# Kernel optimization log

Hardware: AMD Instinct MI355X
Metric: run time of the kernel (lower is better)

## Reference

```python
import jax, jax.numpy as jnp
import numpy as np

B, HIMG, WIMG = 8, 24, 24
WIDTH, NCH, CW = 1024, 8, 128
NHEADS, HD = 8, 16
HALF = HD // 2
NFREQ, VOCAB, NCLS = 32, 256, 10
HIDDEN = 4096
EPS = 1e-6
LAMBDA_INIT = 0.8 - 0.6 * float(np.exp(-0.3 * 0.0))  # layer_idx = 0


def rmsnorm(x, w, eps=EPS):
    return x * jax.lax.rsqrt(jnp.mean(x * x, axis=-1, keepdims=True) + eps) * w


def causal_attn(q, k, v, scale):
    # q,k: [B,H,L,d2], v: [B,H,L,D]
    L = q.shape[2]
    scores = jnp.einsum('bhqd,bhkd->bhqk', q, k) * scale
    mask = jnp.tril(jnp.ones((L, L), dtype=bool))
    scores = jnp.where(mask, scores, -jnp.inf)
    return jnp.einsum('bhqk,bhkd->bhqd', jax.nn.softmax(scores, axis=-1), v)


def diff_attn(h, qkv_w, qkv_b, qn_w, kn_w, hn_w, lq1, lk1, lq2, lk2, ow, ob):
    Bb, L, C = h.shape
    qkv = jax.nn.silu(h @ qkv_w + qkv_b).reshape(Bb, L, 3, NHEADS, HD)
    q, k, v = qkv[:, :, 0], qkv[:, :, 1], qkv[:, :, 2]
    t = lambda a: a.transpose(0, 2, 1, 3)  # [B,L,H,d] -> [B,H,L,d]
    q1 = t(rmsnorm(q[..., :HALF], qn_w)); q2 = t(rmsnorm(q[..., HALF:], qn_w))
    k1 = t(rmsnorm(k[..., :HALF], kn_w)); k2 = t(rmsnorm(k[..., HALF:], kn_w))
    v = t(v)
    lam = jnp.exp(jnp.dot(lq1, lk1)) - jnp.exp(jnp.dot(lq2, lk2)) + LAMBDA_INIT
    scale = 1.0 / np.sqrt(HALF)
    out1 = causal_attn(q1, k1, v, scale)
    out2 = causal_attn(q2, k2, v, scale)
    diff = rmsnorm(out1 - lam * out2, hn_w) * (1.0 - LAMBDA_INIT)
    out = diff.transpose(0, 2, 1, 3).reshape(Bb, L, C)
    return jax.nn.silu(out @ ow + ob)


def setup_inputs() -> dict:
    key = jax.random.key(0)
    ks = iter(jax.random.split(key, 64))
    n = lambda shape, s=0.02: jax.random.normal(next(ks), shape, jnp.float32) * s
    return dict(
        x=jax.random.uniform(next(ks), (B, HIMG, WIMG), jnp.float32),
        top_k=4,
        pixel_embed=n((VOCAB, WIDTH)),
        freq_h=n((NFREQ,), 0.1), freq_w=n((NFREQ,), 0.1),
        phase_h=jnp.zeros((NFREQ,), jnp.float32), phase_w=jnp.zeros((NFREQ,), jnp.float32),
        pos_proj_w=n((4 * NFREQ, WIDTH)), pos_proj_b=jnp.zeros((WIDTH,), jnp.float32),
        embed_norm_w=jnp.ones((WIDTH,), jnp.float32),
        se_w1=n((WIDTH, WIDTH // 4)), se_b1=jnp.zeros((WIDTH // 4,), jnp.float32),
        se_w2=n((WIDTH // 4, WIDTH)), se_b2=jnp.zeros((WIDTH,), jnp.float32),
        mix_norm_w=jnp.ones((WIDTH,), jnp.float32),
        mlp_w1=n((WIDTH, HIDDEN)), mlp_b1=jnp.zeros((HIDDEN,), jnp.float32),
        mlp_w2=n((HIDDEN, WIDTH)), mlp_b2=jnp.zeros((WIDTH,), jnp.float32),
        mlp_norm_w=jnp.ones((WIDTH,), jnp.float32),
        router_w=n((WIDTH, NCH)), router_b=jnp.zeros((NCH,), jnp.float32),
        qkv_w=n((NCH, CW, 3 * CW)), qkv_b=jnp.zeros((NCH, 3 * CW), jnp.float32),
        q_norm_w=jnp.ones((NCH, HALF), jnp.float32), k_norm_w=jnp.ones((NCH, HALF), jnp.float32),
        head_norm_w=jnp.ones((NCH, HD), jnp.float32),
        lam_q1=n((NCH, HALF), 0.1), lam_k1=n((NCH, HALF), 0.1),
        lam_q2=n((NCH, HALF), 0.1), lam_k2=n((NCH, HALF), 0.1),
        out_w=n((NCH, CW, CW)), out_b=jnp.zeros((NCH, CW), jnp.float32),
        seg_norm_w=jnp.ones((NCH, CW), jnp.float32),
        head_w=n((WIDTH, NCLS)), head_b=jnp.zeros((NCLS,), jnp.float32),
    )


def reference(x, top_k, pixel_embed, freq_h, freq_w, phase_h, phase_w, pos_proj_w,
              pos_proj_b, embed_norm_w, se_w1, se_b1, se_w2, se_b2, mix_norm_w,
              mlp_w1, mlp_b1, mlp_w2, mlp_b2, mlp_norm_w, router_w, router_b,
              qkv_w, qkv_b, q_norm_w, k_norm_w, head_norm_w, lam_q1, lam_k1,
              lam_q2, lam_k2, out_w, out_b, seg_norm_w, head_w, head_b):
    Bb, H, W = x.shape
    L = H * W
    # LearnedSinusoidal2DEmbed
    hp = jnp.arange(H, dtype=jnp.float32) / H
    wp = jnp.arange(W, dtype=jnp.float32) / W
    fh = jax.nn.softplus(freq_h) * 10.0
    fw = jax.nn.softplus(freq_w) * 10.0
    ha = hp[:, None] * fh + phase_h          # [H, NFREQ]
    wa = wp[:, None] * fw + phase_w
    h_enc = jnp.concatenate([jnp.sin(ha), jnp.cos(ha)], -1)
    w_enc = jnp.concatenate([jnp.sin(wa), jnp.cos(wa)], -1)
    pos = jnp.concatenate([jnp.broadcast_to(h_enc[:, None], (H, W, 2 * NFREQ)),
                           jnp.broadcast_to(w_enc[None, :], (H, W, 2 * NFREQ))], -1)
    pos = pos @ pos_proj_w + pos_proj_b      # [H, W, WIDTH]
    xi = jnp.clip((x * 255.0).astype(jnp.int32), 0, 255).reshape(Bb, L)
    h = pixel_embed[xi] + pos.reshape(1, L, WIDTH)
    h = rmsnorm(h, embed_norm_w)
    # ChannelMixer: SE + RMSNorm residual, MLP residual, top-k router
    s = jnp.mean(h, axis=1)
    s = jax.nn.sigmoid(jax.nn.silu(s @ se_w1 + se_b1) @ se_w2 + se_b2)
    h = h + rmsnorm(h * s[:, None, :] - h, mix_norm_w)
    h = h + rmsnorm(jax.nn.silu(h @ mlp_w1 + mlp_b1) @ mlp_w2 + mlp_b2, mlp_norm_w)
    logits_r = jnp.mean(h, axis=1) @ router_w + router_b   # [B, NCH]
    tv, ti = jax.lax.top_k(logits_r, top_k)
    rw = jnp.zeros_like(logits_r).at[jnp.arange(Bb)[:, None], ti].set(jax.nn.softmax(tv, axis=-1))
    # ChannelSegment: per-channel differential attention expert, routed
    outs = []
    for i in range(NCH):
        hi = h[..., i * CW:(i + 1) * CW]
        o = diff_attn(hi, qkv_w[i], qkv_b[i], q_norm_w[i], k_norm_w[i], head_norm_w[i],
                      lam_q1[i], lam_k1[i], lam_q2[i], lam_k2[i], out_w[i], out_b[i])
        hi = hi + rmsnorm(o, seg_norm_w[i])
        outs.append(hi * rw[:, i][:, None, None])
    h = jnp.concatenate(outs, axis=-1)
    # classifier head
    return jnp.mean(h, axis=1) @ head_w + head_b
```

## Files before the change

### kernel.cpp

```cpp
#include <hip/hip_runtime.h>
#include <math.h>

typedef __bf16 bf16;
typedef __bf16 bf16x8 __attribute__((ext_vector_type(8)));
typedef __bf16 bf16x4 __attribute__((ext_vector_type(4)));
typedef __bf16 bf16x2 __attribute__((ext_vector_type(2)));
typedef float f32x4 __attribute__((ext_vector_type(4)));
typedef short s16x4 __attribute__((ext_vector_type(4)));

constexpr int Bsz = 8, HIMG = 24, WIMG = 24;
constexpr int Lq = 576;
constexpr int WIDTH = 1024, NCH = 8, CW = 128;
constexpr int NHEADS = 8, HD = 16, HALF = 8;
constexpr float EPS = 1e-6f;
constexpr float LAMINIT = 0.2f;
constexpr float QSCALE_E = 0.35355339059327373f * 1.4426950408889634f;
constexpr int ROWS = Bsz * Lq;

__device__ __forceinline__ float fexp2(float x) {
#if __has_builtin(__builtin_amdgcn_exp2f)
  return __builtin_amdgcn_exp2f(x);
#else
  return exp2f(x);
#endif
}

constexpr size_t B_HB    = 0;
constexpr size_t B_G2B   = B_HB    + 9437184;
constexpr size_t B_ENCB  = B_G2B   + 9437184;
constexpr size_t B_POSWT = B_ENCB  + 163840;
constexpr size_t B_QKVWT = B_POSWT + 262144;
constexpr size_t B_OWT   = B_QKVWT + 786432;
constexpr size_t B_SE    = B_OWT   + 262144;
constexpr size_t B_T1    = B_SE    + 32768;
constexpr size_t B_MP    = B_T1    + 8192;
constexpr size_t B_RW    = B_MP    + 524288;
constexpr size_t B_LAM   = B_RW    + 256;
constexpr size_t B_POOL  = B_LAM   + 256;

__device__ __forceinline__ float blockReduceSum256(float v, float* red) {
  #pragma unroll
  for (int off = 32; off; off >>= 1) v += __shfl_down(v, off, 64);
  int lane = threadIdx.x & 63, wid = threadIdx.x >> 6;
  if (lane == 0) red[wid] = v;
  __syncthreads();
  float total = 0.f;
  #pragma unroll
  for (int i = 0; i < 4; i++) total += red[i];
  return total;
}
__device__ __forceinline__ float silu(float x) { return x / (1.f + __expf(-x)); }

__device__ __forceinline__ void gl16(const bf16* g, bf16* l) {
  __builtin_amdgcn_global_load_lds(
      (const __attribute__((address_space(1))) void*)g,
      (__attribute__((address_space(3))) void*)l, 16, 0, 0);
}

__device__ __forceinline__ f32x4 mfma16(bf16x4 a, bf16x4 b, f32x4 c) {
#if __has_builtin(__builtin_amdgcn_mfma_f32_16x16x16bf16_1k)
  union { bf16x4 h; s16x4 s; } ua, ub;
  ua.h = a; ub.h = b;
  return __builtin_amdgcn_mfma_f32_16x16x16bf16_1k(ua.s, ub.s, c, 0, 0, 0);
#else
  f32x4 d = c;
  asm volatile("v_mfma_f32_16x16x16_bf16 %0, %1, %2, %0"
               : "+v"(d) : "v"(a), "v"(b));
  return d;
#endif
}

__global__ __launch_bounds__(256) void k_tcast(const float* __restrict__ W,
    bf16* __restrict__ Wt, int K, int N) {
  __shared__ float t[32][33];
  int n0 = blockIdx.x * 32, k0 = blockIdx.y * 32;
  long zo = (long)blockIdx.z * K * N;
  int tid = threadIdx.x;
  int r = tid >> 3, c4 = (tid & 7) * 4;
  const float4 v = *(const float4*)(W + zo + (long)(k0 + r) * N + n0 + c4);
  t[c4 + 0][r] = v.x; t[c4 + 1][r] = v.y; t[c4 + 2][r] = v.z; t[c4 + 3][r] = v.w;
  __syncthreads();
  bf16* dst = Wt + zo + (long)(n0 + r) * K + k0 + c4;
  dst[0] = (bf16)t[r][c4 + 0]; dst[1] = (bf16)t[r][c4 + 1];
  dst[2] = (bf16)t[r][c4 + 2]; dst[3] = (bf16)t[r][c4 + 3];
}

__global__ void k_enc_b(const float* __restrict__ fh, const float* __restrict__ fw,
                        const float* __restrict__ ph, const float* __restrict__ pw,
                        bf16* __restrict__ enc) {
  int idx = blockIdx.x * blockDim.x + threadIdx.x;
  if (idx >= Lq * 128) return;
  int l = idx >> 7, c = idx & 127;
  int hh = l / WIMG, ww = l % WIMG;
  float v;
  if (c < 64) {
    int f = c & 31;
    float fr = log1pf(__expf(fh[f])) * 10.f;
    float a = (hh / (float)HIMG) * fr + ph[f];
    v = (c < 32) ? sinf(a) : cosf(a);
  } else {
    int f = c & 31;
    float fr = log1pf(__expf(fw[f])) * 10.f;
    float a = (ww / (float)WIMG) * fr + pw[f];
    v = (c < 96) ? sinf(a) : cosf(a);
  }
  enc[idx] = (bf16)v;
}

template <int ACT, int OUTBF>
__global__ __launch_bounds__(256) void gemm_bt(
    const bf16* __restrict__ A, int lda, long aZs,
    const bf16* __restrict__ Bt, long bZs,
    const float* __restrict__ bias, int biasZs,
    void* __restrict__ Cv, int ldc, long cZs,
    int M, int N, int K) {
  __shared__ bf16 As[128 * 32];
  __shared__ bf16 Bs[128 * 32];
  int tid = threadIdx.x;
  int m0 = blockIdx.y * 128, n0 = blockIdx.x * 128;
  int z = blockIdx.z;
  const bf16* Ab = A + (long)z * aZs;
  const bf16* Bb = Bt + (long)z * bZs;
  f32x4 acc[4][4] = {};
  int wv = tid >> 6, lane = tid & 63;
  int wrow = (wv >> 1) * 64, wcol = (wv & 1) * 64;
  int lm = lane & 15, lq = lane >> 4;
  const bf16* ag = Ab + (long)(m0 + (tid >> 2)) * lda + (tid & 3) * 8;
  const bf16* bg = Bb + (long)(n0 + (tid >> 2)) * K + (tid & 3) * 8;
  bf16* asd = As + tid * 8;
  bf16* bsd = Bs + tid * 8;
  for (int k0 = 0; k0 < K; k0 += 32) {
    gl16(ag + k0, asd);
    gl16(ag + k0 + 64L * lda, asd + 2048);
    gl16(bg + k0, bsd);
    gl16(bg + k0 + 64L * K, bsd + 2048);
    __syncthreads();
    bf16x8 af[4], bfr[4];
    #pragma unroll
    for (int i = 0; i < 4; i++) {
      af[i]  = *(const bf16x8*)(As + (wrow + i * 16 + lm) * 32 + lq * 8);
      bfr[i] = *(const bf16x8*)(Bs + (wcol + i * 16 + lm) * 32 + lq * 8);
    }
    #pragma unroll
    for (int i = 0; i < 4; i++)
      #pragma unroll
      for (int j = 0; j < 4; j++)
        acc[i][j] = __builtin_amdgcn_mfma_f32_16x16x32_bf16(af[i], bfr[j], acc[i][j], 0, 0, 0);
    __syncthreads();
  }
  long cz = (long)z * cZs;
  const float* bz = bias ? bias + (long)z * biasZs : nullptr;
  #pragma unroll
  for (int i = 0; i < 4; i++) {
    int row = m0 + wrow + i * 16 + lq * 4;
    #pragma unroll
    for (int j = 0; j < 4; j++) {
      int col = n0 + wcol + j * 16 + lm;
      float bv = bz ? bz[col] : 0.f;
      #pragma unroll
      for (int r = 0; r < 4; r++) {
        float v = acc[i][j][r] + bv;
        if (ACT == 1) v = silu(v);
        long off = cz + (long)(row + r) * ldc + col;
        if (OUTBF) ((bf16*)Cv)[off] = (bf16)v;
        else       ((float*)Cv)[off] = v;
      }
    }
  }
}

template <int ACT, int OUTBF, int ACC>
__global__ __launch_bounds__(256) void gemm64(
    const bf16* __restrict__ A, int lda, long aZs,
    const bf16* __restrict__ Bt, int ldb, long bZs,
    const float* __restrict__ bias, int biasZs,
    void* __restrict__ Cv, int ldc, long cZs,
    int M, int N, int K) {
  __shared__ bf16 As[64 * 32];
  __shared__ bf16 Bs[128 * 32];
  int tid = threadIdx.x;
  int m0 = blockIdx.y * 64, n0 = blockIdx.x * 128;
  int z = blockIdx.z;
  const bf16* Ab = A + (long)z * aZs;
  const bf16* Bb = Bt + (long)z * bZs;
  f32x4 acc[4][2] = {};
  int wv = tid >> 6, lane = tid & 63;
  int lm = lane & 15, lq = lane >> 4;
  int wcol = wv * 32;
  const bf16* ag = Ab + (long)(m0 + (tid >> 2)) * lda + (tid & 3) * 8;
  const bf16* bg = Bb + (long)(n0 + (tid >> 2)) * ldb + (tid & 3) * 8;
  bf16* asd = As + tid * 8;
  bf16* bsd = Bs + tid * 8;
  for (int k0 = 0; k0 < K; k0 += 32) {
    if (tid < 256) gl16(ag + k0, asd);
    gl16(bg + k0, bsd);
    gl16(bg + k0 + 64L * ldb, bsd + 2048);
    __syncthreads();
    bf16x8 af[4], bfr[2];
    #pragma unroll
    for (int i = 0; i < 4; i++)
      af[i] = *(const bf16x8*)(As + (i * 16 + lm) * 32 + lq * 8);
    #pragma unroll
    for (int j = 0; j < 2; j++)
      bfr[j] = *(const bf16x8*)(Bs + (wcol + j * 16 + lm) * 32 + lq * 8);
    #pragma unroll
    for (int i = 0; i < 4; i++)
      #pragma unroll
      for (int j = 0; j < 2; j++)
        acc[i][j] = __builtin_amdgcn_mfma_f32_16x16x32_bf16(af[i], bfr[j], acc[i][j], 0, 0, 0);
    __syncthreads();
  }
  long cz = (long)z * cZs;
  const float* bz = bias ? bias + (long)z * biasZs : nullptr;
  #pragma unroll
  for (int i = 0; i < 4; i++) {
    int row = m0 + i * 16 + lq * 4;
    #pragma unroll
    for (int j = 0; j < 2; j++) {
      int col = n0 + wcol + j * 16 + lm;
      float bv = bz ? bz[col] : 0.f;
      #pragma unroll
      for (int r = 0; r < 4; r++) {
        float v = acc[i][j][r] + bv;
        long off = cz + (long)(row + r) * ldc + col;
        if (ACC) v += (float)((bf16*)Cv)[off];
        if (ACT == 1) v = silu(v);
        if (OUTBF) ((bf16*)Cv)[off] = (bf16)v;
        else       ((float*)Cv)[off] = v;
      }
    }
  }
}

__global__ __launch_bounds__(256) void k_embed(const float* __restrict__ x,
    const float* __restrict__ emb, const float* __restrict__ pos,
    const float* __restrict__ nw, bf16* __restrict__ h) {
  __shared__ float red[4];
  int row = blockIdx.x;
  int l = row % Lq;
  int xi = (int)(x[row] * 255.f);
  xi = min(max(xi, 0), 255);
  const float* er = emb + (long)xi * WIDTH;
  const float* pr = pos + (long)l * WIDTH;
  int c0 = threadIdx.x * 4;
  float v[4]; float ss = 0.f;
  #pragma unroll
  for (int i = 0; i < 4; i++) { v[i] = er[c0 + i] + pr[c0 + i]; ss += v[i] * v[i]; }
  ss = blockReduceSum256(ss, red);
  float r = rsqrtf(ss / WIDTH + EPS);
  bf16* hr = h + (long)row * WIDTH;
  #pragma unroll
  for (int i = 0; i < 4; i++) hr[c0 + i] = (bf16)(v[i] * r * nw[c0 + i]);
}

__global__ void k_meanl_p(const bf16* __restrict__ h, float* __restrict__ part) {
  int lp = blockIdx.x, b = blockIdx.y, t = threadIdx.x;
  const bf16* p = h + ((long)b * Lq + (long)lp * 36) * WIDTH + t * 4;
  float a0 = 0, a1 = 0, a2 = 0, a3 = 0;
  for (int l = 0; l < 36; l++) {
    bf16x4 v = *(const bf16x4*)(p + (long)l * WIDTH);
    a0 += (float)v[0]; a1 += (float)v[1]; a2 += (float)v[2]; a3 += (float)v[3];
  }
  float* dst = part + ((long)b * 16 + lp) * WIDTH + t * 4;
  dst[0] = a0; dst[1] = a1; dst[2] = a2; dst[3] = a3;
}

__global__ __launch_bounds__(256) void k_se1(const float* __restrict__ part,
    const float* __restrict__ w1, const float* __restrict__ b1,
    float* __restrict__ t1) {
  __shared__ float sv[1024];
  __shared__ float red[256];
  int jb = blockIdx.x, b = blockIdx.y, t = threadIdx.x;
  for (int c = t; c < 1024; c += 256) {
    float a = 0.f;
    #pragma unroll
    for (int lp = 0; lp < 16; lp++) a += part[((long)b * 16 + lp) * 1024 + c];
    sv[c] = a * (1.f / 576.f);
  }
  __syncthreads();
  int j = t & 7, pt = t >> 3;
  int j0 = jb * 8;
  float acc = 0.f;
  int c0 = pt * 32;
  #pragma unroll 8
  for (int c = c0; c < c0 + 32; c++) acc += sv[c] * w1[c * 256 + j0 + j];
  red[t] = acc;
  __syncthreads();
  if (t < 8) {
    float a = b1[j0 + t];
    #pragma unroll
    for (int p = 0; p < 32; p++) a += red[p * 8 + t];
    t1[b * 256 + j0 + t] = silu(a);
  }
}

__global__ __launch_bounds__(256) void k_se2(const float* __restrict__ t1,
    const float* __restrict__ w2, const float* __restrict__ b2,
    float* __restrict__ s) {
  __shared__ float red[256];
  int jb = blockIdx.x, b = blockIdx.y, t = threadIdx.x;
  int j = t & 31, pt = t >> 5;
  int j0 = jb * 32;
  const float* tb = t1 + b * 256;
  float acc = 0.f;
  int c0 = pt * 32;
  #pragma unroll 8
  for (int c = c0; c < c0 + 32; c++) acc += tb[c] * w2[c * 1024 + j0 + j];
  red[t] = acc;
  __syncthreads();
  if (t < 32) {
    float a = b2[j0 + t];
    #pragma unroll
    for (int p = 0; p < 8; p++) a += red[p * 32 + t];
    s[b * 1024 + j0 + t] = 1.f / (1.f + __expf(-a));
  }
}

__global__ __launch_bounds__(256) void k_mix_b(bf16* __restrict__ h,
    const float* __restrict__ s, const float* __restrict__ mw) {
  __shared__ float red[4];
  int row = blockIdx.x;
  int b = row / Lq;
  bf16* hr = h + (long)row * WIDTH;
  const float* sb = s + b * WIDTH;
  int c0 = threadIdx.x * 4;
  float hv[4], y[4]; float ss = 0.f;
  #pragma unroll
  for (int i = 0; i < 4; i++) {
    hv[i] = (float)hr[c0 + i];
    y[i] = hv[i] * (sb[c0 + i] - 1.f); ss += y[i] * y[i];
  }
  ss = blockReduceSum256(ss, red);
  float r = rsqrtf(ss / WIDTH + EPS);
  #pragma unroll
  for (int i = 0; i < 4; i++) hr[c0 + i] = (bf16)(hv[i] + y[i] * r * mw[c0 + i]);
}

__global__ __launch_bounds__(256) void k_addnorm_b(bf16* __restrict__ h,
    const bf16* __restrict__ g, const float* __restrict__ mw) {
  __shared__ float red[4];
  int row = blockIdx.x;
  bf16* hr = h + (long)row * WIDTH;
  const bf16* gr = g + (long)row * WIDTH;
  int c0 = threadIdx.x * 4;
  float y[4]; float ss = 0.f;
  #pragma unroll
  for (int i = 0; i < 4; i++) { y[i] = (float)gr[c0 + i]; ss += y[i] * y[i]; }
  ss = blockReduceSum256(ss, red);
  float r = rsqrtf(ss / WIDTH + EPS);
  #pragma unroll
  for (int i = 0; i < 4; i++)
    hr[c0 + i] = (bf16)((float)hr[c0 + i] + y[i] * r * mw[c0 + i]);
}

__global__ __launch_bounds__(256) void k_router(const float* __restrict__ part,
    const float* __restrict__ rwgt, const float* __restrict__ rb,
    const float* __restrict__ lq1, const float* __restrict__ lk1,
    const float* __restrict__ lq2, const float* __restrict__ lk2,
    float* __restrict__ rw, float* __restrict__ lam) {
  __shared__ float sv[1024];
  __shared__ float red[256];
  __shared__ float lg[8];
  int b = blockIdx.x, t = threadIdx.x;
  for (int c = t; c < 1024; c += 256) {
    float a = 0.f;
    #pragma unroll
    for (int lp = 0; lp < 16; lp++) a += part[((long)b * 16 + lp) * 1024 + c];
    sv[c] = a * (1.f / 576.f);
  }
  __syncthreads();
  int j = t & 7, pt = t >> 3;
  float acc = 0.f;
  int c0 = pt * 32;
  #pragma unroll 8
  for (int c = c0; c < c0 + 32; c++) acc += sv[c] * rwgt[c * 8 + j];
  red[t] = acc;
  __syncthreads();
  if (t < 8) {
    float a = rb[t];
    for (int p = 0; p < 32; p++) a += red[p * 8 + t];
    lg[t] = a;
  }
  __syncthreads();
  if (t == 0) {
    float v[8]; bool sel[8];
    #pragma unroll
    for (int i = 0; i < 8; i++) { v[i] = lg[i]; sel[i] = false; }
    int idxs[4]; float vals[4];
    for (int s = 0; s < 4; s++) {
      int bi = -1; float bv = -1e30f;
      for (int i = 0; i < 8; i++) if (!sel[i] && v[i] > bv) { bv = v[i]; bi = i; }
      sel[bi] = true; idxs[s] = bi; vals[s] = bv;
    }
    float m = vals[0], den = 0.f, e[4];
    for (int s = 0; s < 4; s++) { e[s] = __expf(vals[s] - m); den += e[s]; }
    for (int i = 0; i < 8; i++) rw[b * 8 + i] = 0.f;
    for (int s = 0; s < 4; s++) rw[b * 8 + idxs[s]] = e[s] / den;
  }
  if (b == 0 && t >= 8 && t < 16) {
    int c = t - 8;
    float d1 = 0.f, d2 = 0.f;
    for (int i = 0; i < 8; i++) {
      d1 += lq1[c * 8 + i] * lk1[c * 8 + i];
      d2 += lq2[c * 8 + i] * lk2[c * 8 + i];
    }
    lam[c] = __expf(d1) - __expf(d2) + LAMINIT;
  }
}

__global__ __launch_bounds__(256) void k_attn_mfma(
    const bf16* __restrict__ qkv, const float* __restrict__ lam,
    const float* __restrict__ hnw, const float* __restrict__ qn,
    const float* __restrict__ kn, bf16* __restrict__ dc) {
  __shared__ bf16 Ks[576 * 16];
  __shared__ bf16 Vt[16 * 584];
  int tid = threadIdx.x;
  int slice = blockIdx.x; int zc = slice >> 3, b = slice & 7;
  int head = blockIdx.z;
  const bf16* qkvb = qkv + ((long)zc * ROWS + (long)b * Lq) * 384;
  for (int i = tid; i < 1152; i += 256) {
    int row = i >> 1, hf = i & 1;
    gl16(qkvb + (long)row * 384 + 128 + head * 16 + hf * 8, Ks + i * 8);
  }
  for (int i = tid; i < 1152; i += 256) {
    int row = i >> 1, dh = i & 1;
    bf16x8 v = *(const bf16x8*)(qkvb + (long)row * 384 + 256 + head * 16 + dh * 8);
    #pragma unroll
    for (int j = 0; j < 8; j++) Vt[(dh * 8 + j) * 584 + row] = v[j];
  }
  __syncthreads();
  {
    float kw[8];
    #pragma unroll
    for (int j = 0; j < 8; j++) kw[j] = kn[zc * 8 + j];
    for (int i = tid; i < 1152; i += 256) {
      bf16x8 kv = *(const bf16x8*)(Ks + i * 8);
      float f[8], s = 0.f;
      #pragma unroll
      for (int j = 0; j < 8; j++) { f[j] = (float)kv[j]; s += f[j] * f[j]; }
      float r = rsqrtf(s * 0.125f + EPS);
      bf16x8 o;
      #pragma unroll
      for (int j = 0; j < 8; j++) o[j] = (bf16)(f[j] * r * kw[j]);
      *(bf16x8*)(Ks + i * 8) = o;
    }
  }
  __syncthreads();
  int wv = tid >> 6, lane = tid & 63;
  int lm = lane & 15, lq = lane >> 4;
  float lamv = lam[zc];
  float hwv[4];
  #pragma unroll
  for (int r = 0; r < 4; r++) hwv[r] = hnw[zc * 16 + lq * 4 + r] * (1.f - LAMINIT);
  float qw[8];
  #pragma unroll
  for (int j = 0; j < 8; j++) qw[j] = qn[zc * 8 + j];
  int u = blockIdx.y * 4 + wv;
  int prA, prB, prC;
  if (u < 6) { prA = u + 2; prB = 17 - u; prC = -1; }
  else       { int v2 = u - 6; prA = v2; prB = 8 + v2; prC = 11 - v2; }
  for (int pi = 0; pi < 3; pi++) {
    int pr = (pi == 0) ? prA : (pi == 1) ? prB : prC;
    if (pr < 0) continue;
    bf16x8 bq0[2] = {{}, {}}, bq1[2] = {{}, {}};
    if (lq < 2) {
      #pragma unroll
      for (int tile = 0; tile < 2; tile++) {
        bf16x8 t8 = *(const bf16x8*)(
            qkvb + (long)(pr * 32 + tile * 16 + lm) * 384 + head * 16 + lq * 8);
        float f[8], s = 0.f;
        #pragma unroll
        for (int j = 0; j < 8; j++) { f[j] = (float)t8[j]; s += f[j] * f[j]; }
        float r = rsqrtf(s * 0.125f + EPS) * QSCALE_E;
        bf16x8 n;
        #pragma unroll
        for (int j = 0; j < 8; j++) n[j] = (bf16)(f[j] * r * qw[j]);
        if (lq == 0) bq0[tile] = n; else bq1[tile] = n;
      }
    }
    f32x4 o[2][2] = {};
    float den[2][2] = {};
    for (int kc = 0; kc <= pr; kc++) {
      f32x4 sT[2][2][2] = {};
      #pragma unroll
      for (int t = 0; t < 2; t++) {
        bf16x8 aK = {};
        if (lq < 2) aK = *(const bf16x8*)(Ks + (kc * 32 + t * 16 + lm) * 16 + lq * 8);
        #pragma unroll
        for (int tile = 0; tile < 2; tile++) {
          sT[t][tile][0] = __builtin_amdgcn_mfma_f32_16x16x32_bf16(aK, bq0[tile], sT[t][tile][0], 0, 0, 0);
          sT[t][tile][1] = __builtin_amdgcn_mfma_f32_16x16x32_bf16(aK, bq1[tile], sT[t][tile][1], 0, 0, 0);
        }
      }
      bool diag = (kc == pr);
      #pragma unroll
      for (int t = 0; t < 2; t++) {
        bf16x4 aV = *(const bf16x4*)(Vt + lm * 584 + kc * 32 + t * 16 + lq * 4);
        #pragma unroll
        for (int tile = 0; tile < 2; tile++) {
          if (diag && tile == 0 && t == 1) continue;
          bool masked = diag && (tile == t);
          #pragma unroll
          for (int h2 = 0; h2 < 2; h2++) {
            bf16x4 pb;
            float dsum = 0.f;
            #pragma unroll
            for (int r = 0; r < 4; r++) {
              float ev = fexp2(sT[t][tile][h2][r]);
              if (masked && (lq * 4 + r > lm)) ev = 0.f;
              dsum += ev;
              pb[r] = (bf16)ev;
            }
            den[tile][h2] += dsum;
            o[tile][h2] = mfma16(aV, pb, o[tile][h2]);
          }
        }
      }
    }
    #pragma unroll
    for (int tile = 0; tile < 2; tile++)
      #pragma unroll
      for (int h2 = 0; h2 < 2; h2++) {
        den[tile][h2] += __shfl_xor(den[tile][h2], 16);
        den[tile][h2] += __shfl_xor(den[tile][h2], 32);
      }
    #pragma unroll
    for (int tile = 0; tile < 2; tile++) {
      float inv1 = 1.f / den[tile][0];
      float inv2 = lamv / den[tile][1];
      float dff[4]; float ss = 0.f;
      #pragma unroll
      for (int r = 0; r < 4; r++) {
        dff[r] = o[tile][0][r] * inv1 - o[tile][1][r] * inv2;
        ss += dff[r] * dff[r];
      }
      ss += __shfl_xor(ss, 16);
      ss += __shfl_xor(ss, 32);
      float rr = rsqrtf(ss * 0.0625f + EPS);
      bf16x4 outp;
      #pragma unroll
      for (int r = 0; r < 4; r++) outp[r] = (bf16)(dff[r] * rr * hwv[r]);
      long rowg = (long)zc * ROWS + (long)b * Lq + pr * 32 + tile * 16 + lm;
      *(bf16x4*)(dc + rowg * 128 + head * 16 + lq * 4) = outp;
    }
  }
}

__global__ __launch_bounds__(64) void k_segpool(const bf16* __restrict__ h,
    const bf16* __restrict__ op, const float* __restrict__ segw,
    const float* __restrict__ rw, float* __restrict__ part) {
  int lp = blockIdx.x, b = blockIdx.y, ch = blockIdx.z;
  int t = threadIdx.x;
  int c0 = t * 2;
  float w0 = segw[ch * 128 + c0], w1 = segw[ch * 128 + c0 + 1];
  float rwv = rw[b * 8 + ch];
  float a0 = 0.f, a1 = 0.f;
  for (int l = 0; l < 72; l++) {
    int row = b * Lq + lp * 72 + l;
    const bf16* oprow = op + (long)ch * ROWS * CW + (long)row * CW;
    bf16x2 yv = *(const bf16x2*)(oprow + c0);
    float y0 = (float)yv[0], y1 = (float)yv[1];
    float ss = y0 * y0 + y1 * y1;
    #pragma unroll
    for (int m = 1; m < 64; m <<= 1) ss += __shfl_xor(ss, m);
    float r = rsqrtf(ss * (1.f / 128.f) + EPS);
    bf16x2 hv = *(const bf16x2*)(h + (long)row * WIDTH + ch * 128 + c0);
    a0 += ((float)hv[0] + y0 * r * w0) * rwv;
    a1 += ((float)hv[1] + y1 * r * w1) * rwv;
  }
  float* dst = part + ((long)b * 8 + lp) * 1024 + ch * 128 + c0;
  dst[0] = a0; dst[1] = a1;
}

__global__ __launch_bounds__(256) void k_head(const float* __restrict__ part,
    const float* __restrict__ hw, const float* __restrict__ hb, float* __restrict__ out) {
  __shared__ float pool[1024];
  __shared__ float red[256];
  int b = blockIdx.x, t = threadIdx.x;
  for (int c = t; c < 1024; c += 256) {
    float a = 0.f;
    #pragma unroll
    for (int lp = 0; lp < 8; lp++) a += part[((long)b * 8 + lp) * 1024 + c];
    pool[c] = a * (1.f / 576.f);
  }
  __syncthreads();
  int j = t & 15, pt = t >> 4;
  float acc = 0.f;
  if (j < 10)
    for (int c = pt * 64; c < pt * 64 + 64; c++)
      acc += pool[c] * hw[c * 10 + j];
  red[t] = acc;
  __syncthreads();
  if (t < 10) {
    float a = hb[t];
    for (int p = 0; p < 16; p++) a += red[p * 16 + t];
    out[b * 10 + t] = a;
  }
}

extern "C" void kernel_launch(void* const* d_in, const int* in_sizes, int n_in,
                              void* d_out, int out_size, void* d_ws, size_t ws_size,
                              hipStream_t stream) {
  const float* x          = (const float*)d_in[0];
  const float* pixel_embed= (const float*)d_in[2];
  const float* freq_h     = (const float*)d_in[3];
  const float* freq_w     = (const float*)d_in[4];
  const float* phase_h    = (const float*)d_in[5];
  const float* phase_w    = (const float*)d_in[6];
  const float* pos_proj_w = (const float*)d_in[7];
  const float* pos_proj_b = (const float*)d_in[8];
  const float* embed_norm = (const float*)d_in[9];
  const float* se_w1      = (const float*)d_in[10];
  const float* se_b1      = (const float*)d_in[11];
  const float* se_w2      = (const float*)d_in[12];
  const float* se_b2      = (const float*)d_in[13];
  const float* mix_norm   = (const float*)d_in[14];
  const float* mlp_w1     = (const float*)d_in[15];
  const float* mlp_b1     = (const float*)d_in[16];
  const float* mlp_w2     = (const float*)d_in[17];
  const float* mlp_b2     = (const float*)d_in[18];
  const float* mlp_norm   = (const float*)d_in[19];
  const float* router_w   = (const float*)d_in[20];
  const float* router_b   = (const float*)d_in[21];
  const float* qkv_w      = (const float*)d_in[22];
  const float* qkv_b      = (const float*)d_in[23];
  const float* q_norm_w   = (const float*)d_in[24];
  const float* k_norm_w   = (const float*)d_in[25];
  const float* head_norm_w= (const float*)d_in[26];
  const float* lam_q1     = (const float*)d_in[27];
  const float* lam_k1     = (const float*)d_in[28];
  const float* lam_q2     = (const float*)d_in[29];
  const float* lam_k2     = (const float*)d_in[30];
  const float* out_w      = (const float*)d_in[31];
  const float* out_b      = (const float*)d_in[32];
  const float* seg_norm_w = (const float*)d_in[33];
  const float* head_w     = (const float*)d_in[34];
  const float* head_b     = (const float*)d_in[35];

  char* W = (char*)d_ws;
  bf16*  HB    = (bf16*)(W + B_HB);
  bf16*  G2B   = (bf16*)(W + B_G2B);
  bf16*  ENCB  = (bf16*)(W + B_ENCB);
  bf16*  POSWT = (bf16*)(W + B_POSWT);
  bf16*  QKVWT = (bf16*)(W + B_QKVWT);
  bf16*  OWT   = (bf16*)(W + B_OWT);
  float* SE    = (float*)(W + B_SE);
  float* T1    = (float*)(W + B_T1);
  float* MP    = (float*)(W + B_MP);
  float* RW    = (float*)(W + B_RW);
  float* LAM   = (float*)(W + B_LAM);
  char*  P     = W + B_POOL;
  float* POS   = (float*)P;
  bf16*  W1T   = (bf16*)P;
  bf16*  W2T   = (bf16*)(P + 8388608);
  bf16*  HID   = (bf16*)(P + 16777216);
  bf16*  QKV   = (bf16*)P;
  bf16*  DC    = (bf16*)(P + 28311552);
  float* out   = (float*)d_out;

  k_enc_b<<<288, 256, 0, stream>>>(freq_h, freq_w, phase_h, phase_w, ENCB);
  k_tcast<<<dim3(32, 4, 1), 256, 0, stream>>>(pos_proj_w, POSWT, 128, 1024);
  gemm64<0, 0, 0><<<dim3(8, 10, 1), 256, 0, stream>>>(
      ENCB, 128, 0, POSWT, 128, 0, pos_proj_b, 0, POS, 1024, 0, 640, 1024, 128);
  k_embed<<<ROWS, 256, 0, stream>>>(x, pixel_embed, POS, embed_norm, HB);
  k_meanl_p<<<dim3(16, 8), 256, 0, stream>>>(HB, MP);
  k_se1<<<dim3(32, 8), 256, 0, stream>>>(MP, se_w1, se_b1, T1);
  k_se2<<<dim3(32, 8), 256, 0, stream>>>(T1, se_w2, se_b2, SE);
  k_mix_b<<<ROWS, 256, 0, stream>>>(HB, SE, mix_norm);
  k_tcast<<<dim3(128, 32, 1), 256, 0, stream>>>(mlp_w1, W1T, 1024, 4096);
  k_tcast<<<dim3(32, 128, 1), 256, 0, stream>>>(mlp_w2, W2T, 4096, 1024);
  gemm_bt<1, 1><<<dim3(16, 36, 1), 256, 0, stream>>>(
      HB, 1024, 0, W1T, 0, mlp_b1, 0, HID, 2048, 0, 4608, 2048, 1024);
  gemm64<0, 1, 0><<<dim3(8, 72, 1), 256, 0, stream>>>(
      HID, 2048, 0, W2T, 4096, 0, mlp_b2, 0, G2B, 1024, 0, 4608, 1024, 2048);
  gemm_bt<1, 1><<<dim3(16, 36, 1), 256, 0, stream>>>(
      HB, 1024, 0, W1T + 2048L * 1024, 0, mlp_b1 + 2048, 0, HID, 2048, 0, 4608, 2048, 1024);
  gemm64<0, 1, 1><<<dim3(8, 72, 1), 256, 0, stream>>>(
      HID, 2048, 0, W2T + 2048, 4096, 0, nullptr, 0, G2B, 1024, 0, 4608, 1024, 2048);
  k_addnorm_b<<<ROWS, 256, 0, stream>>>(HB, G2B, mlp_norm);
  k_meanl_p<<<dim3(16, 8), 256, 0, stream>>>(HB, MP);
  k_router<<<8, 256, 0, stream>>>(MP, router_w, router_b,
                                  lam_q1, lam_k1, lam_q2, lam_k2, RW, LAM);
  k_tcast<<<dim3(12, 4, 8), 256, 0, stream>>>(qkv_w, QKVWT, 128, 384);
  k_tcast<<<dim3(4, 4, 8), 256, 0, stream>>>(out_w, OWT, 128, 128);
  gemm64<1, 1, 0><<<dim3(3, 72, 8), 256, 0, stream>>>(
      HB, 1024, CW, QKVWT, 128, 384 * 128, qkv_b, 384,
      QKV, 384, (long)ROWS * 384, ROWS, 384, 128);
  k_attn_mfma<<<dim3(64, 2, 8), 256, 0, stream>>>(
      QKV, LAM, head_norm_w, q_norm_w, k_norm_w, DC);
  gemm64<1, 1, 0><<<dim3(1, 72, 8), 256, 0, stream>>>(
      DC, 128, (long)ROWS * 128, OWT, 128, 128 * 128, out_b, 128,
      DC, 128, (long)ROWS * 128, ROWS, 128, 128);
  k_segpool<<<dim3(8, 8, 8), 64, 0, stream>>>(HB, DC, seg_norm_w, RW, MP);
  k_head<<<8, 256, 0, stream>>>(MP, head_w, head_b, out);
}
```

Measured before the change: 500.7 us.

## Precompute K rmsnorm in separate kernel, read K from global, double attention grid

Measured after the change: 503.3 us. No clear change (+0.5%).

```diff
diff --git a/kernel.cpp b/kernel.cpp
--- a/kernel.cpp
+++ b/kernel.cpp
@@ -408,42 +408,43 @@
   }
 }
 
+__global__ __launch_bounds__(256) void k_knorm(bf16* __restrict__ qkv,
+    const float* __restrict__ kn) {
+  int idx = blockIdx.x * 256 + threadIdx.x;
+  if (idx >= NCH * ROWS * NHEADS) return;
+  int z = idx / (ROWS * NHEADS);
+  int rem = idx - z * (ROWS * NHEADS);
+  int row = rem >> 3, head = rem & 7;
+  bf16* kp = qkv + (long)z * ROWS * 384 + (long)row * 384 + 128 + head * 16;
+  const float* w = kn + z * 8;
+  #pragma unroll
+  for (int hf = 0; hf < 2; hf++) {
+    bf16x8 kv = *(bf16x8*)(kp + hf * 8);
+    float f[8], s = 0.f;
+    #pragma unroll
+    for (int j = 0; j < 8; j++) { f[j] = (float)kv[j]; s += f[j] * f[j]; }
+    float r = rsqrtf(s * 0.125f + EPS);
+    bf16x8 o;
+    #pragma unroll
+    for (int j = 0; j < 8; j++) o[j] = (bf16)(f[j] * r * w[j]);
+    *(bf16x8*)(kp + hf * 8) = o;
+  }
+}
+
 __global__ __launch_bounds__(256) void k_attn_mfma(
     const bf16* __restrict__ qkv, const float* __restrict__ lam,
     const float* __restrict__ hnw, const float* __restrict__ qn,
-    const float* __restrict__ kn, bf16* __restrict__ dc) {
-  __shared__ bf16 Ks[576 * 16];
+    bf16* __restrict__ dc) {
   __shared__ bf16 Vt[16 * 584];
   int tid = threadIdx.x;
   int slice = blockIdx.x; int zc = slice >> 3, b = slice & 7;
   int head = blockIdx.z;
   const bf16* qkvb = qkv + ((long)zc * ROWS + (long)b * Lq) * 384;
   for (int i = tid; i < 1152; i += 256) {
-    int row = i >> 1, hf = i & 1;
-    gl16(qkvb + (long)row * 384 + 128 + head * 16 + hf * 8, Ks + i * 8);
-  }
-  for (int i = tid; i < 1152; i += 256) {
     int row = i >> 1, dh = i & 1;
     bf16x8 v = *(const bf16x8*)(qkvb + (long)row * 384 + 256 + head * 16 + dh * 8);
     #pragma unroll
     for (int j = 0; j < 8; j++) Vt[(dh * 8 + j) * 584 + row] = v[j];
-  }
-  __syncthreads();
-  {
-    float kw[8];
-    #pragma unroll
-    for (int j = 0; j < 8; j++) kw[j] = kn[zc * 8 + j];
-    for (int i = tid; i < 1152; i += 256) {
-      bf16x8 kv = *(const bf16x8*)(Ks + i * 8);
-      float f[8], s = 0.f;
-      #pragma unroll
-      for (int j = 0; j < 8; j++) { f[j] = (float)kv[j]; s += f[j] * f[j]; }
-      float r = rsqrtf(s * 0.125f + EPS);
-      bf16x8 o;
-      #pragma unroll
-      for (int j = 0; j < 8; j++) o[j] = (bf16)(f[j] * r * kw[j]);
-      *(bf16x8*)(Ks + i * 8) = o;
-    }
   }
   __syncthreads();
   int wv = tid >> 6, lane = tid & 63;
@@ -456,11 +457,10 @@
   #pragma unroll
   for (int j = 0; j < 8; j++) qw[j] = qn[zc * 8 + j];
   int u = blockIdx.y * 4 + wv;
-  int prA, prB, prC;
-  if (u < 6) { prA = u + 2; prB = 17 - u; prC = -1; }
-  else       { int v2 = u - 6; prA = v2; prB = 8 + v2; prC = 11 - v2; }
-  for (int pi = 0; pi < 3; pi++) {
-    int pr = (pi == 0) ? prA : (pi == 1) ? prB : prC;
+  int prA = 17 - u;
+  int prB = (u == 15) ? 1 : (u == 14) ? 0 : -1;
+  for (int pi = 0; pi < 2; pi++) {
+    int pr = pi ? prB : prA;
     if (pr < 0) continue;
     bf16x8 bq0[2] = {{}, {}}, bq1[2] = {{}, {}};
     if (lq < 2) {
@@ -485,7 +485,10 @@
       #pragma unroll
       for (int t = 0; t < 2; t++) {
         bf16x8 aK = {};
-        if (lq < 2) aK = *(const bf16x8*)(Ks + (kc * 32 + t * 16 + lm) * 16 + lq * 8);
+        if (lq < 2) {
+          int krow = kc * 32 + t * 16 + lm;
+          aK = *(const bf16x8*)(qkvb + (long)krow * 384 + 128 + head * 16 + lq * 8);
+        }
         #pragma unroll
         for (int tile = 0; tile < 2; tile++) {
           sT[t][tile][0] = __builtin_amdgcn_mfma_f32_16x16x32_bf16(aK, bq0[tile], sT[t][tile][0], 0, 0, 0);
@@ -686,8 +689,9 @@
   gemm64<1, 1, 0><<<dim3(3, 72, 8), 256, 0, stream>>>(
       HB, 1024, CW, QKVWT, 128, 384 * 128, qkv_b, 384,
       QKV, 384, (long)ROWS * 384, ROWS, 384, 128);
-  k_attn_mfma<<<dim3(64, 2, 8), 256, 0, stream>>>(
-      QKV, LAM, head_norm_w, q_norm_w, k_norm_w, DC);
+  k_knorm<<<1152, 256, 0, stream>>>(QKV, k_norm_w);
+  k_attn_mfma<<<dim3(64, 4, 8), 256, 0, stream>>>(
+      QKV, LAM, head_norm_w, q_norm_w, DC);
   gemm64<1, 1, 0><<<dim3(1, 72, 8), 256, 0, stream>>>(
       DC, 128, (long)ROWS * 128, OWT, 128, 128 * 128, out_b, 128,
       DC, 128, (long)ROWS * 128, ROWS, 128, 128);
```
